# Kernel optimization log

Hardware: AMD Instinct MI355X
Metric: run time of the kernel (lower is better)

## Reference

```python
import jax, jax.numpy as jnp
import numpy as np

N = 50000    # total nodes in a batched graph
E = 200000   # directed edges (before self loops)
G = 256      # molecules per batch
F_IN = 64    # atom features
H = 4        # gat heads
CH = 128     # hidden_channels (per head)
D = H * CH   # 512, concat width
MLP_H = 128  # hidden_channels * mlp_hidden_factor
NEG_SLOPE = 0.2


def _gat(x, src, dst, W, a_src, a_dst, b, concat):
    """PyG GATConv (eval mode, self loops already added to src/dst)."""
    n = x.shape[0]
    heads, ch = a_src.shape
    h = (x @ W).reshape(n, heads, ch)                       # [N,H,C]
    e = jax.nn.leaky_relu((h * a_src).sum(-1)[src]
                          + (h * a_dst).sum(-1)[dst], NEG_SLOPE)  # [E,H]
    emax = jax.ops.segment_max(e, dst, num_segments=n)
    emax = jnp.where(jnp.isfinite(emax), emax, 0.0)
    p = jnp.exp(e - emax[dst])
    denom = jax.ops.segment_sum(p, dst, num_segments=n)
    alpha = p / (denom[dst] + 1e-16)                        # segment softmax over dst
    out = jax.ops.segment_sum(h[src] * alpha[..., None], dst, num_segments=n)
    out = out.reshape(n, heads * ch) if concat else out.mean(axis=1)
    return out + b


def _encoder(x, edge_index, batch, p):
    n = x.shape[0]
    loop = jnp.arange(n, dtype=edge_index.dtype)            # GATConv add_self_loops=True
    src = jnp.concatenate([edge_index[0], loop])
    dst = jnp.concatenate([edge_index[1], loop])
    x = jax.nn.elu(_gat(x, src, dst, p['W1'], p['as1'], p['ad1'], p['b1'], True))
    x = jax.nn.elu(_gat(x, src, dst, p['W2'], p['as2'], p['ad2'], p['b2'], True))
    x = _gat(x, src, dst, p['W3'], p['as3'], p['ad3'], p['b3'], False)
    emb = jax.ops.segment_max(x, batch, num_segments=G)     # global_max_pool
    return jnp.where(jnp.isfinite(emb), emb, 0.0)


def setup_inputs() -> dict:
    key = jax.random.key(0)
    ks = jax.random.split(key, 24)
    rn = lambda k, s, sc=0.1: jax.random.normal(k, s, jnp.float32) * sc
    return dict(
        x1=rn(ks[0], (N, F_IN), 1.0),
        edge_index1=jax.random.randint(ks[1], (2, E), 0, N, dtype=jnp.int32),
        batch1=jnp.sort(jax.random.randint(ks[2], (N,), 0, G, dtype=jnp.int32)),
        x2=rn(ks[3], (N, F_IN), 1.0),
        edge_index2=jax.random.randint(ks[4], (2, E), 0, N, dtype=jnp.int32),
        batch2=jnp.sort(jax.random.randint(ks[5], (N,), 0, G, dtype=jnp.int32)),
        W1=rn(ks[6], (F_IN, D)), as1=rn(ks[7], (H, CH)), ad1=rn(ks[8], (H, CH)),
        b1=jnp.zeros((D,), jnp.float32),
        W2=rn(ks[9], (D, D)), as2=rn(ks[10], (H, CH)), ad2=rn(ks[11], (H, CH)),
        b2=jnp.zeros((D,), jnp.float32),
        W3=rn(ks[12], (D, CH)), as3=rn(ks[13], (1, CH)), ad3=rn(ks[14], (1, CH)),
        b3=jnp.zeros((CH,), jnp.float32),
        mw1=rn(ks[15], (2 * CH, MLP_H)), mb1=jnp.zeros((MLP_H,), jnp.float32),
        mw2=rn(ks[16], (MLP_H, 1)), mb2=jnp.zeros((1,), jnp.float32),
    )


def reference(x1, edge_index1, batch1, x2, edge_index2, batch2,
              W1, as1, ad1, b1, W2, as2, ad2, b2, W3, as3, ad3, b3,
              mw1, mb1, mw2, mb2):
    p = dict(W1=W1, as1=as1, ad1=ad1, b1=b1,
             W2=W2, as2=as2, ad2=ad2, b2=b2,
             W3=W3, as3=as3, ad3=ad3, b3=b3)
    e1 = _encoder(x1, edge_index1, batch1, p)               # [G, CH]
    e2 = _encoder(x2, edge_index2, batch2, p)               # [G, CH]
    z = jnp.concatenate([e1, e2], axis=-1)                  # [G, 2*CH]
    return jax.nn.relu(z @ mw1 + mb1) @ mw2 + mb2           # [G, 1]
```

## Files before the change

kernel.cpp:

```cpp
#include <hip/hip_runtime.h>
#include <cstdint>

namespace {
constexpr int kN = 50000;
constexpr int kE = 200000;
constexpr int kE2 = kE + kN;
constexpr int kG = 256;
constexpr float kNegSlope = 0.2f;
}

using half8   = __attribute__((ext_vector_type(8))) _Float16;
using half2v  = __attribute__((ext_vector_type(2))) _Float16;
using floatx4 = __attribute__((ext_vector_type(4))) float;

__device__ __forceinline__ void gld_lds16(const void* g, void* l) {
  __builtin_amdgcn_global_load_lds(
      (const __attribute__((address_space(1))) unsigned int*)g,
      (__attribute__((address_space(3))) unsigned int*)l, 16, 0, 0);
}

__device__ __forceinline__ float fexp(float x) {
  return __builtin_amdgcn_exp2f(x * 1.44269504088896f);
}

template <int OUTF16, int BN, int CT>
__global__ __launch_bounds__(512, 2) void gemm_ring(
    const _Float16* __restrict__ A, const _Float16* __restrict__ B,
    void* __restrict__ Cv, int M, int N, int K) {
  constexpr int ASL = 1024;
  constexpr int BSL = BN * 4;
  constexpr int SLOT = (ASL + BSL) * 16;
  constexpr int LPT = (ASL + BSL) / 512;
  constexpr int WN = (BN == 256) ? 4 : 2;
  constexpr int WM = 8 / WN;
  constexpr int WTM = 256 / WM;
  constexpr int WTN = BN / WN;
  constexpr int MI = WTM / 16;
  constexpr int NI = WTN / 16;
  __shared__ alignas(16) char smem[4 * SLOT];
  const int t = threadIdx.x;
  const int w = t >> 6, l = t & 63;
  const int x = blockIdx.x & 7, s = blockIdx.x >> 3;
  const int col = (CT == 1) ? 0 : (s & (CT - 1));
  const int rt = ((CT == 1) ? s : (s >> 1)) * 8 + x;
  const int bm = rt * 256;
  const int bn = col * BN;
  if (bm >= M) return;
  const int wr = w / WN, wc = w % WN;
  const int quad = l >> 4, lrow = l & 15;

  floatx4 acc[MI][NI];
#pragma unroll
  for (int mi = 0; mi < MI; ++mi)
#pragma unroll
    for (int ni = 0; ni < NI; ++ni) acc[mi][ni] = (floatx4){0.f, 0.f, 0.f, 0.f};

  auto stageA = [&](int kt) {
    char* buf = smem + (size_t)(kt & 3) * SLOT;
    int k0 = kt * 32;
    k0 = (k0 > K - 32) ? (K - 32) : k0;
#pragma unroll
    for (int i = 0; i < 2; ++i) {
      const int sl = i * 512 + t;
      const int row = ((sl >> 6) << 4) + (sl & 15);
      const int q = (sl >> 4) & 3;
      int ga = bm + row;
      ga = (ga < M) ? ga : (M - 1);
      gld_lds16(A + (size_t)ga * K + k0 + q * 8, buf + sl * 16);
    }
  };
  auto stageB = [&](int kt) {
    char* buf = smem + (size_t)(kt & 3) * SLOT + ASL * 16;
    int k0 = kt * 32;
    k0 = (k0 > K - 32) ? (K - 32) : k0;
#pragma unroll
    for (int i = 0; i < LPT - 2; ++i) {
      const int sl = i * 512 + t;
      const int row = ((sl >> 6) << 4) + (sl & 15);
      const int q = (sl >> 4) & 3;
      gld_lds16(B + (size_t)(bn + row) * K + k0 + q * 8, buf + sl * 16);
    }
  };

  stageA(0); stageB(0);
  stageA(1); stageB(1);
  stageA(2); stageB(2);

  const int NT = K >> 5;
  for (int kt = 0; kt < NT; ++kt) {
    char* bufc = smem + (size_t)(kt & 3) * SLOT;
    if constexpr (LPT == 4)
      asm volatile("s_waitcnt vmcnt(8)" ::: "memory");
    else
      asm volatile("s_waitcnt vmcnt(6)" ::: "memory");
    __builtin_amdgcn_s_barrier();
    asm volatile("" ::: "memory");
    stageA(kt + 3);
    half8 fa[MI], fb[NI];
#pragma unroll
    for (int ni = 0; ni < NI; ++ni)
      fb[ni] = *(const half8*)(bufc + ASL * 16 + ((wc * NI + ni) << 10) + l * 16);
#pragma unroll
    for (int mi = 0; mi < MI / 2; ++mi)
      fa[mi] = *(const half8*)(bufc + ((wr * MI + mi) << 10) + l * 16);
    __builtin_amdgcn_s_setprio(1);
#pragma unroll
    for (int mi = 0; mi < MI / 2; ++mi)
#pragma unroll
      for (int ni = 0; ni < NI; ++ni)
        acc[mi][ni] = __builtin_amdgcn_mfma_f32_16x16x32_f16(
            fa[mi], fb[ni], acc[mi][ni], 0, 0, 0);
    __builtin_amdgcn_s_setprio(0);
    stageB(kt + 3);
#pragma unroll
    for (int mi = MI / 2; mi < MI; ++mi)
      fa[mi] = *(const half8*)(bufc + ((wr * MI + mi) << 10) + l * 16);
    __builtin_amdgcn_s_setprio(1);
#pragma unroll
    for (int mi = MI / 2; mi < MI; ++mi)
#pragma unroll
      for (int ni = 0; ni < NI; ++ni)
        acc[mi][ni] = __builtin_amdgcn_mfma_f32_16x16x32_f16(
            fa[mi], fb[ni], acc[mi][ni], 0, 0, 0);
    __builtin_amdgcn_s_setprio(0);
  }
  asm volatile("s_waitcnt vmcnt(0)" ::: "memory");
  const int colbase = bn + wc * WTN + lrow;
#pragma unroll
  for (int mi = 0; mi < MI; ++mi) {
    const int rbase = bm + wr * WTM + mi * 16 + quad * 4;
#pragma unroll
    for (int r = 0; r < 4; ++r) {
      const int grow = rbase + r;
      if (grow < M) {
        if constexpr (OUTF16) {
          _Float16* C = (_Float16*)Cv;
#pragma unroll
          for (int ni = 0; ni < NI; ++ni)
            C[(size_t)grow * N + colbase + ni * 16] = (_Float16)acc[mi][ni][r];
        } else {
          float* C = (float*)Cv;
#pragma unroll
          for (int ni = 0; ni < NI; ++ni)
            C[(size_t)grow * N + colbase + ni * 16] = acc[mi][ni][r];
        }
      }
    }
  }
}

__global__ void wt_split_all(const float* __restrict__ W1, _Float16* Th1,
                             const float* __restrict__ W2, _Float16* Th2,
                             const float* __restrict__ W3, _Float16* Th3) {
  int idx = blockIdx.x * blockDim.x + threadIdx.x;
  const float* W;
  _Float16* Th;
  int K, N;
  if (idx < 64 * 512) {
    W = W1; Th = Th1; K = 64; N = 512;
  } else if (idx < 64 * 512 + 512 * 512) {
    idx -= 64 * 512;
    W = W2; Th = Th2; K = 512; N = 512;
  } else if (idx < 64 * 512 + 512 * 512 + 512 * 128) {
    idx -= 64 * 512 + 512 * 512;
    W = W3; Th = Th3; K = 512; N = 128;
  } else {
    return;
  }
  const int k = idx / N;
  const int n = idx - k * N;
  Th[n * K + k] = (_Float16)W[idx];
}

__global__ void prep_all(const float* __restrict__ x0, const float* __restrict__ x1,
                         _Float16* __restrict__ Xh, int* __restrict__ cnt,
                         int* __restrict__ total,
                         const float* __restrict__ W1, _Float16* Th1,
                         const float* __restrict__ W2, _Float16* Th2,
                         const float* __restrict__ W3, _Float16* Th3) {
  const int idx = blockIdx.x * blockDim.x + threadIdx.x;
  const int half = kN * 64;
  if (idx < half) {
    Xh[idx] = (_Float16)x0[idx];
  } else if (idx < 2 * half) {
    Xh[idx] = (_Float16)x1[idx - half];
  } else {
    int e = idx - 2 * half;
    const float* W;
    _Float16* Th;
    int K, N;
    if (e < 64 * 512) {
      W = W1; Th = Th1; K = 64; N = 512;
    } else if (e < 64 * 512 + 512 * 512) {
      e -= 64 * 512;
      W = W2; Th = Th2; K = 512; N = 512;
    } else if (e < 64 * 512 + 512 * 512 + 512 * 128) {
      e -= 64 * 512 + 512 * 512;
      W = W3; Th = Th3; K = 512; N = 128;
    } else {
      W = nullptr; Th = nullptr; K = N = 0;
    }
    if (W) {
      const int k = e / N;
      const int n = e - k * N;
      Th[n * K + k] = (_Float16)W[e];
    }
  }
  if (idx < 2 * kN) cnt[idx] = 1;
  if (idx == 0) *total = 0;
}
__global__ void prep(const float* __restrict__ X, _Float16* __restrict__ Xh,
                     int* __restrict__ cnt, int* __restrict__ total, int nsplit,
                     int n) {
  const int idx = blockIdx.x * blockDim.x + threadIdx.x;
  if (idx < nsplit) Xh[idx] = (_Float16)X[idx];
  if (idx < n) cnt[idx] = 1;
  if (idx == 0) *total = 0;
}

__global__ void count_edges2(const int* __restrict__ d0, const int* __restrict__ d1,
                             int* __restrict__ cnt) {
  const int i = blockIdx.x * blockDim.x + threadIdx.x;
  if (i < kE) atomicAdd(&cnt[d0[i]], 1);
  else if (i < 2 * kE) atomicAdd(&cnt[d1[i - kE] + kN], 1);
}
__global__ void fill_edges2(const int* __restrict__ s0, const int* __restrict__ d0,
                            const int* __restrict__ s1, const int* __restrict__ d1,
                            int* __restrict__ cursor, int* __restrict__ csr) {
  const int i = blockIdx.x * blockDim.x + threadIdx.x;
  if (i < kE) {
    const int p = atomicAdd(&cursor[d0[i]], 1);
    csr[p] = s0[i];
  } else if (i < 2 * kE) {
    const int j = i - kE;
    const int p = atomicAdd(&cursor[d1[j] + kN], 1);
    csr[p] = s1[j] + kN;
  }
}
__global__ void count_edges(const int* __restrict__ dst, int* __restrict__ cnt,
                            int ne) {
  const int i = blockIdx.x * blockDim.x + threadIdx.x;
  if (i < ne) atomicAdd(&cnt[dst[i]], 1);
}
__global__ void fill_edges(const int* __restrict__ src, const int* __restrict__ dst,
                           int* __restrict__ cursor, int* __restrict__ csr, int ne) {
  const int i = blockIdx.x * blockDim.x + threadIdx.x;
  if (i < ne) {
    const int p = atomicAdd(&cursor[dst[i]], 1);
    csr[p] = src[i];
  }
}
__global__ void alloc_ranges(const int* __restrict__ cnt, int* __restrict__ start,
                             int* __restrict__ cursor, int* __restrict__ total,
                             int* __restrict__ csr, int n) {
  const int i = blockIdx.x * blockDim.x + threadIdx.x;
  const int lane = threadIdx.x & 63;
  const int v = (i < n) ? cnt[i] : 0;
  int sc = v;
#pragma unroll
  for (int off = 1; off < 64; off <<= 1) {
    const int t = __shfl_up(sc, off);
    if (lane >= off) sc += t;
  }
  const int wtot = __shfl(sc, 63);
  int base = 0;
  if (lane == 63) base = atomicAdd(total, wtot);
  base = __shfl(base, 63);
  const int st = base + sc - v;
  if (i < n) {
    start[i] = st;
    cursor[i] = st + 1;
    csr[st] = i;
  }
}

__global__ void gat_agg4(const _Float16* __restrict__ h,
                         const float* __restrict__ a_src,
                         const float* __restrict__ a_dst,
                         const int* __restrict__ start, const int* __restrict__ cnt,
                         const int* __restrict__ csr_src,
                         const float* __restrict__ bias,
                         _Float16* __restrict__ outH, int n_nodes) {
  const int gtid = blockIdx.x * blockDim.x + threadIdx.x;
  const int wid = gtid >> 6;
  const int lane = threadIdx.x & 63;
  const int n0 = wid * 2;
  if (n0 >= n_nodes) return;
  const int n1r = (n0 + 1 < n_nodes) ? (n0 + 1) : n0;
  const bool has1 = (n0 + 1 < n_nodes);
  const int ch = lane * 8;
  float as_r[8], ad_r[8];
#pragma unroll
  for (int j = 0; j < 8; ++j) {
    as_r[j] = a_src[ch + j];
    ad_r[j] = a_dst[ch + j];
  }
  const int s0 = start[n0], c0 = cnt[n0];
  const int s1 = start[n1r];
  const int c1 = has1 ? cnt[n1r] : 0;
  const half8 vsA = *(const half8*)(h + (size_t)n0 * 512 + ch);
  const half8 vsB = *(const half8*)(h + (size_t)n1r * 512 + ch);
  float fsA[8], fsB[8];
  float tAs = 0.f, tAd = 0.f, tBs = 0.f, tBd = 0.f;
#pragma unroll
  for (int j = 0; j < 8; ++j) {
    fsA[j] = (float)vsA[j];
    fsB[j] = (float)vsB[j];
    tAs = fmaf(fsA[j], as_r[j], tAs);
    tAd = fmaf(fsA[j], ad_r[j], tAd);
    tBs = fmaf(fsB[j], as_r[j], tBs);
    tBd = fmaf(fsB[j], ad_r[j], tBd);
  }
#pragma unroll
  for (int off = 1; off < 16; off <<= 1) {
    tAs += __shfl_xor(tAs, off);
    tAd += __shfl_xor(tAd, off);
    tBs += __shfl_xor(tBs, off);
    tBd += __shfl_xor(tBd, off);
  }
  const float adA = tAd, adB = tBd;
  float eA = tAs + adA, eB = tBs + adB;
  eA = (eA > 0.f) ? eA : kNegSlope * eA;
  eB = (eB > 0.f) ? eB : kNegSlope * eB;
  const float wsA = fexp(eA);
  const float wsB = fexp(eB);
  float dA = wsA, dB = wsB;
  float aA[8], aB[8];
#pragma unroll
  for (int j = 0; j < 8; ++j) {
    aA[j] = wsA * fsA[j];
    aB[j] = wsB * fsB[j];
  }
  const int cm = (c0 > c1) ? c0 : c1;
  int i = 1;
  for (; i + 2 <= cm; i += 2) {
    const int jA0 = (i < c0) ? i : 0, jA1 = (i + 1 < c0) ? i + 1 : 0;
    const int jB0 = (i < c1) ? i : 0, jB1 = (i + 1 < c1) ? i + 1 : 0;
    const int sA0 = csr_src[s0 + jA0];
    const int sA1 = csr_src[s0 + jA1];
    const int sB0 = csr_src[s1 + jB0];
    const int sB1 = csr_src[s1 + jB1];
    const half8 vA0 = *(const half8*)(h + (size_t)sA0 * 512 + ch);
    const half8 vA1 = *(const half8*)(h + (size_t)sA1 * 512 + ch);
    const half8 vB0 = *(const half8*)(h + (size_t)sB0 * 512 + ch);
    const half8 vB1 = *(const half8*)(h + (size_t)sB1 * 512 + ch);
    float fA0[8], fA1[8], fB0[8], fB1[8];
    float tA0 = 0.f, tA1 = 0.f, tB0 = 0.f, tB1 = 0.f;
#pragma unroll
    for (int j = 0; j < 8; ++j) {
      fA0[j] = (float)vA0[j]; tA0 = fmaf(fA0[j], as_r[j], tA0);
      fA1[j] = (float)vA1[j]; tA1 = fmaf(fA1[j], as_r[j], tA1);
      fB0[j] = (float)vB0[j]; tB0 = fmaf(fB0[j], as_r[j], tB0);
      fB1[j] = (float)vB1[j]; tB1 = fmaf(fB1[j], as_r[j], tB1);
    }
#pragma unroll
    for (int off = 1; off < 16; off <<= 1) {
      tA0 += __shfl_xor(tA0, off);
      tA1 += __shfl_xor(tA1, off);
      tB0 += __shfl_xor(tB0, off);
      tB1 += __shfl_xor(tB1, off);
    }
    float eA0 = tA0 + adA, eA1 = tA1 + adA;
    float eB0 = tB0 + adB, eB1 = tB1 + adB;
    eA0 = (eA0 > 0.f) ? eA0 : kNegSlope * eA0;
    eA1 = (eA1 > 0.f) ? eA1 : kNegSlope * eA1;
    eB0 = (eB0 > 0.f) ? eB0 : kNegSlope * eB0;
    eB1 = (eB1 > 0.f) ? eB1 : kNegSlope * eB1;
    const float wA0 = (i < c0) ? fexp(eA0) : 0.f;
    const float wA1 = (i + 1 < c0) ? fexp(eA1) : 0.f;
    const float wB0 = (i < c1) ? fexp(eB0) : 0.f;
    const float wB1 = (i + 1 < c1) ? fexp(eB1) : 0.f;
    dA += wA0 + wA1;
    dB += wB0 + wB1;
#pragma unroll
    for (int j = 0; j < 8; ++j) {
      aA[j] = fmaf(wA0, fA0[j], aA[j]);
      aA[j] = fmaf(wA1, fA1[j], aA[j]);
      aB[j] = fmaf(wB0, fB0[j], aB[j]);
      aB[j] = fmaf(wB1, fB1[j], aB[j]);
    }
  }
  if (i < cm) {
    const int jA = (i < c0) ? i : 0;
    const int jB = (i < c1) ? i : 0;
    const int sA = csr_src[s0 + jA];
    const int sB = csr_src[s1 + jB];
    const half8 vA = *(const half8*)(h + (size_t)sA * 512 + ch);
    const half8 vB = *(const half8*)(h + (size_t)sB * 512 + ch);
    float fA[8], fB[8];
    float tA = 0.f, tB = 0.f;
#pragma unroll
    for (int j = 0; j < 8; ++j) {
      fA[j] = (float)vA[j]; tA = fmaf(fA[j], as_r[j], tA);
      fB[j] = (float)vB[j]; tB = fmaf(fB[j], as_r[j], tB);
    }
#pragma unroll
    for (int off = 1; off < 16; off <<= 1) {
      tA += __shfl_xor(tA, off);
      tB += __shfl_xor(tB, off);
    }
    float eA2 = tA + adA, eB2 = tB + adB;
    eA2 = (eA2 > 0.f) ? eA2 : kNegSlope * eA2;
    eB2 = (eB2 > 0.f) ? eB2 : kNegSlope * eB2;
    const float wA = (i < c0) ? fexp(eA2) : 0.f;
    const float wB = (i < c1) ? fexp(eB2) : 0.f;
    dA += wA;
    dB += wB;
#pragma unroll
    for (int j = 0; j < 8; ++j) {
      aA[j] = fmaf(wA, fA[j], aA[j]);
      aB[j] = fmaf(wB, fB[j], aB[j]);
    }
  }
  const float invA = 1.f / (dA + 1e-16f);
  const float invB = 1.f / (dB + 1e-16f);
  half8 HA, HB;
#pragma unroll
  for (int j = 0; j < 8; ++j) {
    float vA = aA[j] * invA + bias[ch + j];
    vA = (vA > 0.f) ? vA : (fexp(vA) - 1.f);
    HA[j] = (_Float16)vA;
    float vB = aB[j] * invB + bias[ch + j];
    vB = (vB > 0.f) ? vB : (fexp(vB) - 1.f);
    HB[j] = (_Float16)vB;
  }
  *(half8*)(outH + (size_t)n0 * 512 + ch) = HA;
  if (has1) *(half8*)(outH + (size_t)n1r * 512 + ch) = HB;
}

__global__ void gat_agg_l3(const _Float16* __restrict__ h,
                           const float* __restrict__ a_src,
                           const float* __restrict__ a_dst,
                           const int* __restrict__ start, const int* __restrict__ cnt,
                           const int* __restrict__ csr_src,
                           const float* __restrict__ bias,
                           float* __restrict__ out, int n_nodes) {
  const int gtid = blockIdx.x * blockDim.x + threadIdx.x;
  const int wid = gtid >> 6;
  const int lane = threadIdx.x & 63;
  const int n0 = wid * 2;
  if (n0 >= n_nodes) return;
  const int n1r = (n0 + 1 < n_nodes) ? (n0 + 1) : n0;
  const bool has1 = (n0 + 1 < n_nodes);
  const float2 asv = *(const float2*)(a_src + lane * 2);
  const float2 adv = *(const float2*)(a_dst + lane * 2);
  const int s0 = start[n0], c0 = cnt[n0];
  const int s1 = start[n1r];
  const int c1 = has1 ? cnt[n1r] : 0;
  const half2v vsA = *(const half2v*)(h + (size_t)n0 * 128 + lane * 2);
  const half2v vsB = *(const half2v*)(h + (size_t)n1r * 128 + lane * 2);
  const float xA = (float)vsA[0], yA = (float)vsA[1];
  const float xB = (float)vsB[0], yB = (float)vsB[1];
  float tAs = fmaf(xA, asv.x, yA * asv.y);
  float tAd = fmaf(xA, adv.x, yA * adv.y);
  float tBs = fmaf(xB, asv.x, yB * asv.y);
  float tBd = fmaf(xB, adv.x, yB * adv.y);
#pragma unroll
  for (int off = 1; off < 64; off <<= 1) {
    tAs += __shfl_xor(tAs, off);
    tAd += __shfl_xor(tAd, off);
    tBs += __shfl_xor(tBs, off);
    tBd += __shfl_xor(tBd, off);
  }
  const float adA = tAd, adB = tBd;
  float eA = tAs + adA, eB = tBs + adB;
  eA = (eA > 0.f) ? eA : kNegSlope * eA;
  eB = (eB > 0.f) ? eB : kNegSlope * eB;
  const float wsA = fexp(eA);
  const float wsB = fexp(eB);
  float dA = wsA, dB = wsB;
  float2 aA = make_float2(wsA * xA, wsA * yA);
  float2 aB = make_float2(wsB * xB, wsB * yB);
  const int cm = (c0 > c1) ? c0 : c1;
  int i = 1;
  for (; i + 2 <= cm; i += 2) {
    const int jA0 = (i < c0) ? i : 0, jA1 = (i + 1 < c0) ? i + 1 : 0;
    const int jB0 = (i < c1) ? i : 0, jB1 = (i + 1 < c1) ? i + 1 : 0;
    const int sA0 = csr_src[s0 + jA0];
    const int sA1 = csr_src[s0 + jA1];
    const int sB0 = csr_src[s1 + jB0];
    const int sB1 = csr_src[s1 + jB1];
    const half2v vA0 = *(const half2v*)(h + (size_t)sA0 * 128 + lane * 2);
    const half2v vA1 = *(const half2v*)(h + (size_t)sA1 * 128 + lane * 2);
    const half2v vB0 = *(const half2v*)(h + (size_t)sB0 * 128 + lane * 2);
    const half2v vB1 = *(const half2v*)(h + (size_t)sB1 * 128 + lane * 2);
    const float xA0 = (float)vA0[0], yA0 = (float)vA0[1];
    const float xA1 = (float)vA1[0], yA1 = (float)vA1[1];
    const float xB0 = (float)vB0[0], yB0 = (float)vB0[1];
    const float xB1 = (float)vB1[0], yB1 = (float)vB1[1];
    float tA0 = fmaf(xA0, asv.x, yA0 * asv.y);
    float tA1 = fmaf(xA1, asv.x, yA1 * asv.y);
    float tB0 = fmaf(xB0, asv.x, yB0 * asv.y);
    float tB1 = fmaf(xB1, asv.x, yB1 * asv.y);
#pragma unroll
    for (int off = 1; off < 64; off <<= 1) {
      tA0 += __shfl_xor(tA0, off);
      tA1 += __shfl_xor(tA1, off);
      tB0 += __shfl_xor(tB0, off);
      tB1 += __shfl_xor(tB1, off);
    }
    float eA0 = tA0 + adA, eA1 = tA1 + adA;
    float eB0 = tB0 + adB, eB1 = tB1 + adB;
    eA0 = (eA0 > 0.f) ? eA0 : kNegSlope * eA0;
    eA1 = (eA1 > 0.f) ? eA1 : kNegSlope * eA1;
    eB0 = (eB0 > 0.f) ? eB0 : kNegSlope * eB0;
    eB1 = (eB1 > 0.f) ? eB1 : kNegSlope * eB1;
    const float wA0 = (i < c0) ? fexp(eA0) : 0.f;
    const float wA1 = (i + 1 < c0) ? fexp(eA1) : 0.f;
    const float wB0 = (i < c1) ? fexp(eB0) : 0.f;
    const float wB1 = (i + 1 < c1) ? fexp(eB1) : 0.f;
    dA += wA0 + wA1;
    dB += wB0 + wB1;
    aA.x = fmaf(wA0, xA0, aA.x); aA.x = fmaf(wA1, xA1, aA.x);
    aA.y = fmaf(wA0, yA0, aA.y); aA.y = fmaf(wA1, yA1, aA.y);
    aB.x = fmaf(wB0, xB0, aB.x); aB.x = fmaf(wB1, xB1, aB.x);
    aB.y = fmaf(wB0, yB0, aB.y); aB.y = fmaf(wB1, yB1, aB.y);
  }
  if (i < cm) {
    const int jA = (i < c0) ? i : 0;
    const int jB = (i < c1) ? i : 0;
    const int sA = csr_src[s0 + jA];
    const int sB = csr_src[s1 + jB];
    const half2v vA = *(const half2v*)(h + (size_t)sA * 128 + lane * 2);
    const half2v vB = *(const half2v*)(h + (size_t)sB * 128 + lane * 2);
    const float xA2 = (float)vA[0], yA2 = (float)vA[1];
    const float xB2 = (float)vB[0], yB2 = (float)vB[1];
    float tA = fmaf(xA2, asv.x, yA2 * asv.y);
    float tB = fmaf(xB2, asv.x, yB2 * asv.y);
#pragma unroll
    for (int off = 1; off < 64; off <<= 1) {
      tA += __shfl_xor(tA, off);
      tB += __shfl_xor(tB, off);
    }
    float eA2 = tA + adA, eB2 = tB + adB;
    eA2 = (eA2 > 0.f) ? eA2 : kNegSlope * eA2;
    eB2 = (eB2 > 0.f) ? eB2 : kNegSlope * eB2;
    const float wA = (i < c0) ? fexp(eA2) : 0.f;
    const float wB = (i < c1) ? fexp(eB2) : 0.f;
    dA += wA;
    dB += wB;
    aA.x = fmaf(wA, xA2, aA.x);
    aA.y = fmaf(wA, yA2, aA.y);
    aB.x = fmaf(wB, xB2, aB.x);
    aB.y = fmaf(wB, yB2, aB.y);
  }
  const float invA = 1.f / (dA + 1e-16f);
  const float invB = 1.f / (dB + 1e-16f);
  *(float2*)(out + (size_t)n0 * 128 + lane * 2) =
      make_float2(aA.x * invA + bias[lane * 2],
                  aA.y * invA + bias[lane * 2 + 1]);
  if (has1)
    *(float2*)(out + (size_t)n1r * 128 + lane * 2) =
        make_float2(aB.x * invB + bias[lane * 2],
                    aB.y * invB + bias[lane * 2 + 1]);
}

__global__ void pool_max2(const float* __restrict__ x, const int* __restrict__ bt1,
                          const int* __restrict__ bt2, float* __restrict__ emb) {
  __shared__ int lohi[2];
  const int enc = blockIdx.x >> 8;
  const int g = blockIdx.x & 255;
  const int* batch = enc ? bt2 : bt1;
  const float* xx = x + (size_t)enc * kN * 128;
  if (threadIdx.x == 0) {
    int lo = 0, hi = kN;
    while (lo < hi) {
      const int mid = (lo + hi) >> 1;
      if (batch[mid] < g) lo = mid + 1; else hi = mid;
    }
    lohi[0] = lo;
    hi = kN;
    while (lo < hi) {
      const int mid = (lo + hi) >> 1;
      if (batch[mid] < g + 1) lo = mid + 1; else hi = mid;
    }
    lohi[1] = lo;
  }
  __syncthreads();
  const int lo = lohi[0], hi = lohi[1];
  const int c = threadIdx.x;
  float m = -1e30f;
  for (int nid = lo; nid < hi; ++nid) m = fmaxf(m, xx[(size_t)nid * 128 + c]);
  emb[(size_t)blockIdx.x * 128 + c] = (lo < hi) ? m : 0.f;
}
__global__ void pool_max(const float* __restrict__ x, const int* __restrict__ batch,
                         float* __restrict__ emb, int n_nodes) {
  __shared__ int lohi[2];
  const int g = blockIdx.x;
  if (threadIdx.x == 0) {
    int lo = 0, hi = n_nodes;
    while (lo < hi) {
      const int mid = (lo + hi) >> 1;
      if (batch[mid] < g) lo = mid + 1; else hi = mid;
    }
    lohi[0] = lo;
    hi = n_nodes;
    while (lo < hi) {
      const int mid = (lo + hi) >> 1;
      if (batch[mid] < g + 1) lo = mid + 1; else hi = mid;
    }
    lohi[1] = lo;
  }
  __syncthreads();
  const int lo = lohi[0], hi = lohi[1];
  const int c = threadIdx.x;
  float m = -1e30f;
  for (int nid = lo; nid < hi; ++nid) m = fmaxf(m, x[(size_t)nid * 128 + c]);
  emb[g * 128 + c] = (lo < hi) ? m : 0.f;
}

__global__ void mlp_head(const float* __restrict__ e1, const float* __restrict__ e2,
                         const float* __restrict__ mw1, const float* __restrict__ mb1,
                         const float* __restrict__ mw2, const float* __restrict__ mb2,
                         float* __restrict__ out) {
  __shared__ float z[256];
  __shared__ float red[128];
  const int g = blockIdx.x;
  const int j = threadIdx.x;
  z[j] = e1[g * 128 + j];
  z[j + 128] = e2[g * 128 + j];
  __syncthreads();
  float acc = mb1[j];
  for (int k = 0; k < 256; ++k) acc = fmaf(z[k], mw1[k * 128 + j], acc);
  acc = fmaxf(acc, 0.f) * mw2[j];
  red[j] = acc;
  __syncthreads();
  for (int s = 64; s > 0; s >>= 1) {
    if (j < s) red[j] += red[j + s];
    __syncthreads();
  }
  if (j == 0) out[g] = red[0] + mb2[0];
}

namespace {
struct Bufs {
  _Float16 *R1h, *R2h;
  float *R1f, *R2f, *asrc, *adst;
  int *cnt, *start, *cursor, *csr, *total;
  _Float16 *Wth1, *Wth2, *Wth3;
  float* emb;
  size_t need;
};

Bufs plan(void* d_ws, int M, int E) {
  Bufs b;
  char* w = (char*)d_ws;
  size_t off = 0;
  auto take = [&](size_t bytes) -> void* {
    void* p = w + off;
    off += (bytes + 255) & ~(size_t)255;
    return p;
  };
  b.R1h = (_Float16*)take((size_t)M * 512 * 2);
  b.R1f = (float*)b.R1h;
  b.R2h = (_Float16*)take((size_t)M * 512 * 2);
  b.R2f = (float*)b.R2h;
  b.asrc = (float*)take((size_t)M * 4 * 4);
  b.adst = (float*)take((size_t)M * 4 * 4);
  b.cnt = (int*)take((size_t)M * 4);
  b.start = (int*)take((size_t)M * 4);
  b.cursor = (int*)take((size_t)M * 4);
  b.csr = (int*)take((size_t)E * 4);
  b.total = (int*)take(256);
  b.Wth1 = (_Float16*)take((size_t)64 * 512 * 2);
  b.Wth2 = (_Float16*)take((size_t)512 * 512 * 2);
  b.Wth3 = (_Float16*)take((size_t)512 * 128 * 2);
  b.emb = (float*)take((size_t)2 * kG * 128 * 4);
  b.need = off;
  return b;
}

void run_layers(const Bufs& b, void* const* d_in, int M, hipStream_t stream) {
  const float* as1 = (const float*)d_in[7];
  const float* ad1 = (const float*)d_in[8];
  const float* b1 = (const float*)d_in[9];
  const float* as2 = (const float*)d_in[11];
  const float* ad2 = (const float*)d_in[12];
  const float* b2 = (const float*)d_in[13];
  const float* as3 = (const float*)d_in[15];
  const float* ad3 = (const float*)d_in[16];
  const float* b3 = (const float*)d_in[17];
  const int aggBlocks = (((M + 1) / 2) * 64 + 255) / 256;
  const int MT = (M + 255) / 256;
  const int SP = (MT + 7) / 8;

  gemm_ring<1, 256, 2><<<SP * 16, 512, 0, stream>>>(b.R1h, b.Wth1, b.R2h, M, 512, 64);
  gat_agg4<<<aggBlocks, 256, 0, stream>>>(b.R2h, as1, ad1, b.start, b.cnt,
                                          b.csr, b1, b.R1h, M);
  gemm_ring<1, 256, 2><<<SP * 16, 512, 0, stream>>>(b.R1h, b.Wth2, b.R2h, M, 512, 512);
  gat_agg4<<<aggBlocks, 256, 0, stream>>>(b.R2h, as2, ad2, b.start, b.cnt,
                                          b.csr, b2, b.R1h, M);
  gemm_ring<1, 128, 1><<<SP * 8, 512, 0, stream>>>(b.R1h, b.Wth3, b.R2h, M, 128, 512);
  gat_agg_l3<<<aggBlocks, 256, 0, stream>>>(b.R2h, as3, ad3, b.start, b.cnt,
                                            b.csr, b3, b.R1f, M);
}
}

extern "C" void kernel_launch(void* const* d_in, const int* in_sizes, int n_in,
                              void* d_out, int out_size, void* d_ws, size_t ws_size,
                              hipStream_t stream) {
  (void)in_sizes; (void)n_in; (void)out_size;
  const float* W1 = (const float*)d_in[6];
  const float* W2 = (const float*)d_in[10];
  const float* W3 = (const float*)d_in[14];
  const float* mw1 = (const float*)d_in[18];
  const float* mb1 = (const float*)d_in[19];
  const float* mw2 = (const float*)d_in[20];
  const float* mb2 = (const float*)d_in[21];

  Bufs bc = plan(d_ws, 2 * kN, 2 * kE2);
  const bool combined = bc.need <= ws_size;
  Bufs b = combined ? bc : plan(d_ws, kN, kE2);

  const int wtot = 64 * 512 + 512 * 512 + 512 * 128;
  if (combined) {
    const int M = 2 * kN;
    const int* ei0 = (const int*)d_in[1];
    const int* ei1 = (const int*)d_in[4];
    prep_all<<<(M * 64 + wtot + 255) / 256, 256, 0, stream>>>(
        (const float*)d_in[0], (const float*)d_in[3], b.R1h, b.cnt, b.total,
        W1, b.Wth1, W2, b.Wth2, W3, b.Wth3);
    count_edges2<<<(2 * kE + 255) / 256, 256, 0, stream>>>(ei0 + kE, ei1 + kE,
                                                           b.cnt);
    alloc_ranges<<<(M + 255) / 256, 256, 0, stream>>>(b.cnt, b.start, b.cursor,
                                                      b.total, b.csr, M);
    fill_edges2<<<(2 * kE + 255) / 256, 256, 0, stream>>>(ei0, ei0 + kE, ei1,
                                                          ei1 + kE, b.cursor, b.csr);
    run_layers(b, d_in, M, stream);
    pool_max2<<<2 * kG, 128, 0, stream>>>(b.R1f, (const int*)d_in[2],
                                          (const int*)d_in[5], b.emb);
  } else {
    wt_split_all<<<(wtot + 255) / 256, 256, 0, stream>>>(W1, b.Wth1, W2, b.Wth2,
                                                         W3, b.Wth3);
    for (int enc = 0; enc < 2; ++enc) {
      const float* x = (const float*)d_in[enc * 3 + 0];
      const int* ei = (const int*)d_in[enc * 3 + 1];
      const int* batch = (const int*)d_in[enc * 3 + 2];
      prep<<<(kN * 64 + 255) / 256, 256, 0, stream>>>(x, b.R1h, b.cnt, b.total,
                                                      kN * 64, kN);
      count_edges<<<(kE + 255) / 256, 256, 0, stream>>>(ei + kE, b.cnt, kE);
      alloc_ranges<<<(kN + 255) / 256, 256, 0, stream>>>(b.cnt, b.start, b.cursor,
                                                         b.total, b.csr, kN);
      fill_edges<<<(kE + 255) / 256, 256, 0, stream>>>(ei, ei + kE, b.cursor, b.csr,
                                                       kE);
      run_layers(b, d_in, kN, stream);
      pool_max<<<kG, 128, 0, stream>>>(b.R1f, batch, b.emb + (size_t)enc * kG * 128,
                                       kN);
    }
  }
  mlp_head<<<kG, 128, 0, stream>>>(b.emb, b.emb + (size_t)kG * 128, mw1, mb1, mw2,
                                   mb2, (float*)d_out);
}
```

Baseline: 635.3 us.

## Shrink GEMM tiles to 128-row blocks with 256 threads and triple-buffered ring

The fp16 MFMA GEMM now uses 128-row M tiles with 4 waves of 256 threads instead of 256-row tiles with 8 waves. Its shared-memory ring drops from four slots to three, with prefetch depth two, and the vmcnt waits and slot indexing are adjusted to match. The intent is to cut LDS footprint and create more blocks so the GPU is better filled and occupancy rises. In exchange each block reuses operand data less and the prefetch pipeline is shallower, which may expose more memory latency.

```diff
diff --git a/kernel.cpp b/kernel.cpp
--- a/kernel.cpp
+++ b/kernel.cpp
@@ -24,29 +24,27 @@
 }
 
 template <int OUTF16, int BN, int CT>
-__global__ __launch_bounds__(512, 2) void gemm_ring(
+__global__ __launch_bounds__(256, 2) void gemm_ring(
     const _Float16* __restrict__ A, const _Float16* __restrict__ B,
     void* __restrict__ Cv, int M, int N, int K) {
-  constexpr int ASL = 1024;
+  constexpr int ASL = 512;
   constexpr int BSL = BN * 4;
   constexpr int SLOT = (ASL + BSL) * 16;
-  constexpr int LPT = (ASL + BSL) / 512;
-  constexpr int WN = (BN == 256) ? 4 : 2;
-  constexpr int WM = 8 / WN;
-  constexpr int WTM = 256 / WM;
-  constexpr int WTN = BN / WN;
+  constexpr int LPT = (ASL + BSL) / 256;
+  constexpr int WTM = 64;
+  constexpr int WTN = BN / 2;
   constexpr int MI = WTM / 16;
   constexpr int NI = WTN / 16;
-  __shared__ alignas(16) char smem[4 * SLOT];
+  __shared__ alignas(16) char smem[3 * SLOT];
   const int t = threadIdx.x;
   const int w = t >> 6, l = t & 63;
   const int x = blockIdx.x & 7, s = blockIdx.x >> 3;
   const int col = (CT == 1) ? 0 : (s & (CT - 1));
   const int rt = ((CT == 1) ? s : (s >> 1)) * 8 + x;
-  const int bm = rt * 256;
+  const int bm = rt * 128;
   const int bn = col * BN;
   if (bm >= M) return;
-  const int wr = w / WN, wc = w % WN;
+  const int wr = w >> 1, wc = w & 1;
   const int quad = l >> 4, lrow = l & 15;
 
   floatx4 acc[MI][NI];
@@ -55,13 +53,13 @@
 #pragma unroll
     for (int ni = 0; ni < NI; ++ni) acc[mi][ni] = (floatx4){0.f, 0.f, 0.f, 0.f};
 
-  auto stageA = [&](int kt) {
-    char* buf = smem + (size_t)(kt & 3) * SLOT;
+  auto stageA = [&](int slot, int kt) {
+    char* buf = smem + (size_t)slot * SLOT;
     int k0 = kt * 32;
     k0 = (k0 > K - 32) ? (K - 32) : k0;
 #pragma unroll
-    for (int i = 0; i < 2; ++i) {
-      const int sl = i * 512 + t;
+    for (int i = 0; i < ASL / 256; ++i) {
+      const int sl = i * 256 + t;
       const int row = ((sl >> 6) << 4) + (sl & 15);
       const int q = (sl >> 4) & 3;
       int ga = bm + row;
@@ -69,33 +67,34 @@
       gld_lds16(A + (size_t)ga * K + k0 + q * 8, buf + sl * 16);
     }
   };
-  auto stageB = [&](int kt) {
-    char* buf = smem + (size_t)(kt & 3) * SLOT + ASL * 16;
+  auto stageB = [&](int slot, int kt) {
+    char* buf = smem + (size_t)slot * SLOT + ASL * 16;
     int k0 = kt * 32;
     k0 = (k0 > K - 32) ? (K - 32) : k0;
 #pragma unroll
-    for (int i = 0; i < LPT - 2; ++i) {
-      const int sl = i * 512 + t;
+    for (int i = 0; i < BSL / 256; ++i) {
+      const int sl = i * 256 + t;
       const int row = ((sl >> 6) << 4) + (sl & 15);
       const int q = (sl >> 4) & 3;
       gld_lds16(B + (size_t)(bn + row) * K + k0 + q * 8, buf + sl * 16);
     }
   };
 
-  stageA(0); stageB(0);
-  stageA(1); stageB(1);
-  stageA(2); stageB(2);
+  stageA(0, 0); stageB(0, 0);
+  stageA(1, 1); stageB(1, 1);
 
   const int NT = K >> 5;
+  int cur = 0;
   for (int kt = 0; kt < NT; ++kt) {
-    char* bufc = smem + (size_t)(kt & 3) * SLOT;
-    if constexpr (LPT == 4)
-      asm volatile("s_waitcnt vmcnt(8)" ::: "memory");
+    char* bufc = smem + (size_t)cur * SLOT;
+    const int stg = (cur == 0) ? 2 : (cur - 1);
+    if constexpr (LPT == 6)
+      asm volatile("s_waitcnt vmcnt(6)" ::: "memory");
     else
-      asm volatile("s_waitcnt vmcnt(6)" ::: "memory");
+      asm volatile("s_waitcnt vmcnt(4)" ::: "memory");
     __builtin_amdgcn_s_barrier();
     asm volatile("" ::: "memory");
-    stageA(kt + 3);
+    stageA(stg, kt + 2);
     half8 fa[MI], fb[NI];
 #pragma unroll
     for (int ni = 0; ni < NI; ++ni)
@@ -111,7 +110,7 @@
         acc[mi][ni] = __builtin_amdgcn_mfma_f32_16x16x32_f16(
             fa[mi], fb[ni], acc[mi][ni], 0, 0, 0);
     __builtin_amdgcn_s_setprio(0);
-    stageB(kt + 3);
+    stageB(stg, kt + 2);
 #pragma unroll
     for (int mi = MI / 2; mi < MI; ++mi)
       fa[mi] = *(const half8*)(bufc + ((wr * MI + mi) << 10) + l * 16);
@@ -123,6 +122,7 @@
         acc[mi][ni] = __builtin_amdgcn_mfma_f32_16x16x32_f16(
             fa[mi], fb[ni], acc[mi][ni], 0, 0, 0);
     __builtin_amdgcn_s_setprio(0);
+    cur = (cur == 2) ? 0 : (cur + 1);
   }
   asm volatile("s_waitcnt vmcnt(0)" ::: "memory");
   const int colbase = bn + wc * WTN + lrow;
@@ -681,16 +681,16 @@
   const float* ad3 = (const float*)d_in[16];
   const float* b3 = (const float*)d_in[17];
   const int aggBlocks = (((M + 1) / 2) * 64 + 255) / 256;
-  const int MT = (M + 255) / 256;
-  const int SP = (MT + 7) / 8;
-
-  gemm_ring<1, 256, 2><<<SP * 16, 512, 0, stream>>>(b.R1h, b.Wth1, b.R2h, M, 512, 64);
+  const int RT = (M + 127) / 128;
+  const int SP = (RT + 7) / 8;
+
+  gemm_ring<1, 256, 2><<<SP * 16, 256, 0, stream>>>(b.R1h, b.Wth1, b.R2h, M, 512, 64);
   gat_agg4<<<aggBlocks, 256, 0, stream>>>(b.R2h, as1, ad1, b.start, b.cnt,
                                           b.csr, b1, b.R1h, M);
-  gemm_ring<1, 256, 2><<<SP * 16, 512, 0, stream>>>(b.R1h, b.Wth2, b.R2h, M, 512, 512);
+  gemm_ring<1, 256, 2><<<SP * 16, 256, 0, stream>>>(b.R1h, b.Wth2, b.R2h, M, 512, 512);
   gat_agg4<<<aggBlocks, 256, 0, stream>>>(b.R2h, as2, ad2, b.start, b.cnt,
                                           b.csr, b2, b.R1h, M);
-  gemm_ring<1, 128, 1><<<SP * 8, 512, 0, stream>>>(b.R1h, b.Wth3, b.R2h, M, 128, 512);
+  gemm_ring<1, 128, 1><<<SP * 8, 256, 0, stream>>>(b.R1h, b.Wth3, b.R2h, M, 128, 512);
   gat_agg_l3<<<aggBlocks, 256, 0, stream>>>(b.R2h, as3, ad3, b.start, b.cnt,
                                             b.csr, b3, b.R1f, M);
 }
```

Result: no change. 633.2 us (-0.3%).
